# Performance work log

Hardware: AMD Instinct MI355X
Metric: run time of the kernel (lower is better)

## Reference

```python
import jax, jax.numpy as jnp
import numpy as np

NUM_PAPERS = 500000
NUM_AUTHORS = 200000
NUM_EDGES = 2000000
NUM_LABEL_EDGES = 500000
FEAT = 128
HID = 128


def setup_inputs() -> dict:
    key = jax.random.key(0)
    ks = jax.random.split(key, 9)
    paper_x = jax.random.normal(ks[0], (NUM_PAPERS, FEAT), dtype=jnp.float32)
    author_ids = jax.random.randint(ks[1], (NUM_EDGES,), 0, NUM_AUTHORS, dtype=jnp.int32)
    paper_ids = jax.random.randint(ks[2], (NUM_EDGES,), 0, NUM_PAPERS, dtype=jnp.int32)
    label_author_ids = jax.random.randint(ks[3], (NUM_LABEL_EDGES,), 0, NUM_AUTHORS, dtype=jnp.int32)
    label_paper_ids = jax.random.randint(ks[4], (NUM_LABEL_EDGES,), 0, NUM_PAPERS, dtype=jnp.int32)
    s = 1.0 / np.sqrt(FEAT)
    W_paper = jax.random.normal(ks[5], (FEAT, HID), dtype=jnp.float32) * s
    b_paper = jax.random.normal(ks[6], (HID,), dtype=jnp.float32) * 0.01
    W_author = jax.random.normal(ks[7], (HID, HID), dtype=jnp.float32) * s
    b_author = jax.random.normal(ks[8], (HID,), dtype=jnp.float32) * 0.01
    return {
        'paper_x': paper_x,
        'author_ids': author_ids,
        'paper_ids': paper_ids,
        'label_author_ids': label_author_ids,
        'label_paper_ids': label_paper_ids,
        'W_paper': W_paper,
        'b_paper': b_paper,
        'W_author': W_author,
        'b_author': b_author,
    }


def reference(paper_x, author_ids, paper_ids, label_author_ids, label_paper_ids,
              W_paper, b_paper, W_author, b_author):
    # lin_paper: [num_papers, feat] @ [feat, hid] + bias
    paper_h = paper_x @ W_paper + b_paper
    # gather paper embeddings along 'writes' edges: [num_edges, hid]
    gathered = paper_h[paper_ids]
    # scatter_mean over author ids -> [num_authors, hid]
    sums = jax.ops.segment_sum(gathered, author_ids, num_segments=NUM_AUTHORS)
    counts = jax.ops.segment_sum(jnp.ones((author_ids.shape[0],), dtype=paper_h.dtype),
                                 author_ids, num_segments=NUM_AUTHORS)
    author_h = sums / jnp.maximum(counts, 1.0)[:, None]  # authors with no papers -> 0
    # lin_author
    author_h = author_h @ W_author + b_author
    # Classifier: edgewise dot product on supervision edges -> [num_label_edges]
    pred = jnp.sum(author_h[label_author_ids] * paper_h[label_paper_ids], axis=-1)
    return pred
```

## Files before the change

### kernel.cpp

```cpp
#include <hip/hip_runtime.h>

typedef __attribute__((ext_vector_type(8))) short short8;
typedef __attribute__((ext_vector_type(8))) unsigned short ushort8;
typedef __attribute__((ext_vector_type(4))) unsigned short ushort4_t;
typedef __attribute__((ext_vector_type(4))) float floatx4;

#define NUM_AUTHORS 200000
#define HID 128
#define ABITS 9
#define NB 391
#define CHUNK 8192
#define TPB 32
#define OSTRIDE 136

__device__ __forceinline__ unsigned short f32_to_bf16(float f) {
  union { float f; unsigned int u; } v; v.f = f;
  unsigned int u = v.u;
  u += 0x7FFF + ((u >> 16) & 1);
  return (unsigned short)(u >> 16);
}
__device__ __forceinline__ float bf16_to_f32(unsigned short h) {
  union { unsigned int u; float f; } v; v.u = ((unsigned int)h) << 16; return v.f;
}

__global__ __launch_bounds__(256) void prep_w(
    const float* __restrict__ Wp, const float* __restrict__ Wa,
    unsigned short* __restrict__ WtP, unsigned short* __restrict__ WtA)
{
  const float* W = blockIdx.x ? Wa : Wp;
  unsigned short* Wt = blockIdx.x ? WtA : WtP;
  int t = threadIdx.x;
#pragma unroll
  for (int i = 0; i < 8; ++i) {
    int idx = i * 256 + t;
    int f = idx >> 6;
    int lane = idx & 63;
    int tt = f >> 2, ks = f & 3;
    int m = lane & 15, q = lane >> 4;
    int col = tt * 16 + m;
    int kb = ks * 32 + q * 8;
    ushort8 h;
#pragma unroll
    for (int j = 0; j < 8; ++j) h[j] = f32_to_bf16(W[(size_t)(kb + j) * HID + col]);
    *(ushort8*)&Wt[(size_t)idx * 8] = h;
  }
}

template<bool X_IS_BF16>
__global__ __launch_bounds__(256, 4) void gemm_mfma(
    const void* __restrict__ Xv, const unsigned short* __restrict__ Wfrag,
    const float* __restrict__ bias, const int* __restrict__ counts,
    unsigned short* __restrict__ Y, int M, int nTiles)
{
  __shared__ unsigned short Bs[32 * 64 * 8];
  __shared__ unsigned short Obuf[4 * 16 * OSTRIDE];
  const int t = threadIdx.x;
#pragma unroll
  for (int i = 0; i < 8; ++i) {
    int g = i * 256 + t;
    *(ushort8*)&Bs[(size_t)g * 8] = *(const ushort8*)&Wfrag[(size_t)g * 8];
  }
  __syncthreads();

  const int w = t >> 6;
  const int lane = t & 63;
  const int m = lane & 15;
  const int q = lane >> 4;
  unsigned short* ob = &Obuf[w * 16 * OSTRIDE];

  const int tileBase = blockIdx.x * TPB;

#pragma unroll 1
  for (int i = 0; i < TPB / 4; ++i) {
    const int tile = tileBase + i * 4 + w;
    if (tile >= nTiles) break;
    const int p = tile * 16 + m;
    const bool valid = (p < M);

    short8 xf[4];
    if (X_IS_BF16) {
      const unsigned short* X = (const unsigned short*)Xv;
      const unsigned short* xp = X + (size_t)p * HID + q * 8;
#pragma unroll
      for (int ks = 0; ks < 4; ++ks) {
        if (valid) xf[ks] = *(const short8*)(xp + ks * 32);
        else       xf[ks] = (short8)0;
      }
    } else {
      const float* X = (const float*)Xv;
      const float* xp = X + (size_t)p * HID + q * 8;
#pragma unroll
      for (int ks = 0; ks < 4; ++ks) {
        float4 a0, a1;
        if (valid) {
          a0 = *(const float4*)(xp + ks * 32);
          a1 = *(const float4*)(xp + ks * 32 + 4);
        } else {
          a0 = make_float4(0.f, 0.f, 0.f, 0.f); a1 = a0;
        }
        short8 h;
        h[0] = (short)f32_to_bf16(a0.x); h[1] = (short)f32_to_bf16(a0.y);
        h[2] = (short)f32_to_bf16(a0.z); h[3] = (short)f32_to_bf16(a0.w);
        h[4] = (short)f32_to_bf16(a1.x); h[5] = (short)f32_to_bf16(a1.y);
        h[6] = (short)f32_to_bf16(a1.z); h[7] = (short)f32_to_bf16(a1.w);
        xf[ks] = h;
      }
    }

    floatx4 acc[8];
#pragma unroll
    for (int tt = 0; tt < 8; ++tt) acc[tt] = (floatx4)(0.f);

#pragma unroll
    for (int ks = 0; ks < 4; ++ks) {
#pragma unroll
      for (int tt = 0; tt < 8; ++tt) {
        short8 wf = *(const short8*)&Bs[(size_t)((tt * 4 + ks) * 64 + lane) * 8];
        acc[tt] = __builtin_amdgcn_mfma_f32_16x16x32_bf16(wf, xf[ks], acc[tt], 0, 0, 0);
      }
    }

    float inv = 1.0f;
    if (counts) {
      float c = valid ? (float)counts[p] : 1.0f;
      inv = 1.0f / fmaxf(c, 1.0f);
    }

#pragma unroll
    for (int tt = 0; tt < 8; ++tt) {
      const float4 bv = *(const float4*)(bias + tt * 16 + q * 4);
      ushort4_t o;
      o[0] = f32_to_bf16(acc[tt][0] * inv + bv.x);
      o[1] = f32_to_bf16(acc[tt][1] * inv + bv.y);
      o[2] = f32_to_bf16(acc[tt][2] * inv + bv.z);
      o[3] = f32_to_bf16(acc[tt][3] * inv + bv.w);
      *(ushort4_t*)&ob[m * OSTRIDE + tt * 16 + q * 4] = o;
    }
    asm volatile("s_waitcnt lgkmcnt(0)" ::: "memory");

    {
      const int r = lane & 15;
      const int c = lane >> 4;
      const int row = tile * 16 + r;
#pragma unroll
      for (int j = 0; j < 4; ++j) {
        ushort8 v = *(const ushort8*)&ob[r * OSTRIDE + j * 32 + c * 8];
        if (row < M)
          *(ushort8*)(Y + (size_t)row * HID + j * 32 + c * 8) = v;
      }
    }
    asm volatile("s_waitcnt lgkmcnt(0)" ::: "memory");
  }
}

__global__ __launch_bounds__(256) void hist_kernel(
    const int* __restrict__ aid, int* __restrict__ cnt, int n)
{
  int i = blockIdx.x * 256 + threadIdx.x;
  if (i < n) atomicAdd(&cnt[aid[i]], 1);
}

__global__ __launch_bounds__(256) void scan1(
    const int* __restrict__ cnt, int* __restrict__ offsets,
    int* __restrict__ blockSums, int n)
{
  __shared__ int s[256];
  int t = threadIdx.x;
  int i = blockIdx.x * 256 + t;
  int v = (i < n) ? cnt[i] : 0;
  s[t] = v; __syncthreads();
#pragma unroll
  for (int off = 1; off < 256; off <<= 1) {
    int tv = 0;
    if (t >= off) tv = s[t - off];
    __syncthreads();
    if (t >= off) s[t] += tv;
    __syncthreads();
  }
  if (i < n) offsets[i] = s[t] - v;
  if (t == 255) blockSums[blockIdx.x] = s[255];
}

__global__ __launch_bounds__(1024) void scan2(int* __restrict__ blockSums, int nb)
{
  __shared__ int s[1024];
  int t = threadIdx.x;
  int v = (t < nb) ? blockSums[t] : 0;
  s[t] = v; __syncthreads();
#pragma unroll
  for (int off = 1; off < 1024; off <<= 1) {
    int tv = 0;
    if (t >= off) tv = s[t - off];
    __syncthreads();
    if (t >= off) s[t] += tv;
    __syncthreads();
  }
  if (t < nb) blockSums[t] = s[t] - v;
}

__global__ __launch_bounds__(256) void scan3(
    int* __restrict__ offsets, const int* __restrict__ blockSums, int n)
{
  int i = blockIdx.x * 256 + threadIdx.x;
  if (i < n) offsets[i] += blockSums[blockIdx.x];
}

__global__ __launch_bounds__(256) void bucket_hist(
    const int* __restrict__ aid, int* __restrict__ bcnt, int n)
{
  __shared__ int hist[NB];
  int t = threadIdx.x;
  for (int i = t; i < NB; i += 256) hist[i] = 0;
  __syncthreads();
  int e0 = blockIdx.x * CHUNK;
  int e1 = min(e0 + CHUNK, n);
  for (int e = e0 + t; e < e1; e += 256) atomicAdd(&hist[aid[e] >> ABITS], 1);
  __syncthreads();
  for (int i = t; i < NB; i += 256) {
    int h = hist[i];
    if (h) atomicAdd(&bcnt[i], h);
  }
}

__global__ __launch_bounds__(512) void bucket_scan(
    const int* __restrict__ bcnt, int* __restrict__ boff, int* __restrict__ bcur, int n)
{
  __shared__ int s[512];
  int t = threadIdx.x;
  int v = (t < NB) ? bcnt[t] : 0;
  s[t] = v; __syncthreads();
#pragma unroll
  for (int off = 1; off < 512; off <<= 1) {
    int tv = 0;
    if (t >= off) tv = s[t - off];
    __syncthreads();
    if (t >= off) s[t] += tv;
    __syncthreads();
  }
  if (t < NB) { int e = s[t] - v; boff[t] = e; bcur[t] = e; }
  if (t == 0) boff[NB] = n;
}

__global__ __launch_bounds__(256) void partA(
    const int* __restrict__ aid, const int* __restrict__ pid,
    int* __restrict__ bcur, uint2* __restrict__ pairs, int n)
{
  __shared__ int hist[NB];
  __shared__ int cur[NB];
  int t = threadIdx.x;
  for (int i = t; i < NB; i += 256) hist[i] = 0;
  __syncthreads();
  int e0 = blockIdx.x * CHUNK;
  int e1 = min(e0 + CHUNK, n);
  for (int e = e0 + t; e < e1; e += 256) atomicAdd(&hist[aid[e] >> ABITS], 1);
  __syncthreads();
  for (int i = t; i < NB; i += 256) {
    int h = hist[i];
    cur[i] = h ? atomicAdd(&bcur[i], h) : 0;
  }
  __syncthreads();
  for (int e = e0 + t; e < e1; e += 256) {
    int a = aid[e];
    int pos = atomicAdd(&cur[a >> ABITS], 1);
    pairs[pos] = make_uint2((unsigned)a, (unsigned)pid[e]);
  }
}

__global__ __launch_bounds__(256) void partB(
    const uint2* __restrict__ pairs, const int* __restrict__ boff,
    const int* __restrict__ offsets, int* __restrict__ csr)
{
  __shared__ int lcur[1 << ABITS];
  int b = blockIdx.x;
  int t = threadIdx.x;
  int a0 = b << ABITS;
  for (int i = t; i < (1 << ABITS); i += 256) {
    int g = a0 + i;
    lcur[i] = (g < NUM_AUTHORS) ? offsets[g] : 0;
  }
  __syncthreads();
  int s = boff[b], e = boff[b + 1];
  for (int i = s + t; i < e; i += 256) {
    uint2 pr = pairs[i];
    int pos = atomicAdd(&lcur[pr.x - a0], 1);
    csr[pos] = (int)pr.y;
  }
}

__global__ __launch_bounds__(256) void accumulate_kernel(
    const unsigned short* __restrict__ paper_hb, const int* __restrict__ csr,
    const int* __restrict__ offsets, const int* __restrict__ cnt,
    unsigned short* __restrict__ author_in)
{
  int a = blockIdx.x * 4 + (threadIdx.x >> 6);
  if (a >= NUM_AUTHORS) return;
  int lane = threadIdx.x & 63;
  int sub = lane >> 4;
  int c16 = lane & 15;
  int start = offsets[a];
  int n = cnt[a];
  float acc[8];
#pragma unroll
  for (int j = 0; j < 8; ++j) acc[j] = 0.f;
  for (int i = 0; i < n; i += 4) {
    int idx = i + sub;
    if (idx < n) {
      int p = csr[start + idx];
      ushort8 h = *(const ushort8*)(paper_hb + (size_t)p * HID + c16 * 8);
#pragma unroll
      for (int j = 0; j < 8; ++j) acc[j] += bf16_to_f32(h[j]);
    }
  }
#pragma unroll
  for (int j = 0; j < 8; ++j) {
    acc[j] += __shfl_xor(acc[j], 16, 64);
    acc[j] += __shfl_xor(acc[j], 32, 64);
  }
  if (sub == 0) {
    ushort8 o;
#pragma unroll
    for (int j = 0; j < 8; ++j) o[j] = f32_to_bf16(acc[j]);
    *(ushort8*)(author_in + (size_t)a * HID + c16 * 8) = o;
  }
}

__global__ __launch_bounds__(256) void dot_kernel(
    const unsigned short* __restrict__ author_hb, const unsigned short* __restrict__ paper_hb,
    const int* __restrict__ la, const int* __restrict__ lp,
    float* __restrict__ out, int n)
{
  int e = blockIdx.x * 16 + (threadIdx.x >> 4);
  if (e >= n) return;
  int c16 = threadIdx.x & 15;
  int a = la[e], p = lp[e];
  ushort8 ah = *(const ushort8*)(author_hb + (size_t)a * HID + c16 * 8);
  ushort8 ph = *(const ushort8*)(paper_hb + (size_t)p * HID + c16 * 8);
  float s = 0.f;
#pragma unroll
  for (int j = 0; j < 8; ++j) s += bf16_to_f32(ah[j]) * bf16_to_f32(ph[j]);
  s += __shfl_xor(s, 1, 64);
  s += __shfl_xor(s, 2, 64);
  s += __shfl_xor(s, 4, 64);
  s += __shfl_xor(s, 8, 64);
  if (c16 == 0) out[e] = s;
}

extern "C" void kernel_launch(void* const* d_in, const int* in_sizes, int n_in,
                              void* d_out, int out_size, void* d_ws, size_t ws_size,
                              hipStream_t stream)
{
  const float* paper_x          = (const float*)d_in[0];
  const int*   author_ids       = (const int*)d_in[1];
  const int*   paper_ids        = (const int*)d_in[2];
  const int*   label_author_ids = (const int*)d_in[3];
  const int*   label_paper_ids  = (const int*)d_in[4];
  const float* W_paper          = (const float*)d_in[5];
  const float* b_paper          = (const float*)d_in[6];
  const float* W_author         = (const float*)d_in[7];
  const float* b_author         = (const float*)d_in[8];
  float* out = (float*)d_out;

  const int num_papers = in_sizes[0] / HID;
  const int num_edges  = in_sizes[1];
  const int num_label  = in_sizes[3];
  const int NA = NUM_AUTHORS;

  char* ws = (char*)d_ws;
  size_t off = 0;
  auto alloc = [&](size_t bytes) { void* p = ws + off; off = (off + bytes + 255) & ~(size_t)255; return p; };
  unsigned short* paper_hb  = (unsigned short*)alloc((size_t)num_papers * HID * 2);
  unsigned short* author_in = (unsigned short*)alloc((size_t)NA * HID * 2);
  unsigned short* author_hb = (unsigned short*)alloc((size_t)NA * HID * 2);
  int* counts_int = (int*)alloc((size_t)NA * 4);
  int* bcnt       = (int*)alloc((size_t)(NB + 1) * 4);
  int* boff       = (int*)alloc((size_t)(NB + 1) * 4);
  int* bcur       = (int*)alloc((size_t)NB * 4);
  int* offsets    = (int*)alloc((size_t)NA * 4);
  int* blockSums  = (int*)alloc(1024 * 4);
  int* csr        = (int*)alloc((size_t)num_edges * 4);
  uint2* pairs    = (uint2*)alloc((size_t)num_edges * 8);
  unsigned short* WtP = (unsigned short*)alloc(HID * HID * 2);
  unsigned short* WtA = (unsigned short*)alloc(HID * HID * 2);

  hipMemsetAsync(counts_int, 0, (size_t)NA * 4, stream);
  hipMemsetAsync(bcnt, 0, (size_t)(NB + 1) * 4, stream);

  prep_w<<<2, 256, 0, stream>>>(W_paper, W_author, WtP, WtA);

  {
    const int nTiles = (num_papers + 15) / 16;
    const int blocks = (nTiles + TPB - 1) / TPB;
    gemm_mfma<false><<<blocks, 256, 0, stream>>>(
        paper_x, WtP, b_paper, nullptr, paper_hb, num_papers, nTiles);
  }

  hist_kernel<<<(num_edges + 255) / 256, 256, 0, stream>>>(author_ids, counts_int, num_edges);

  const int nb = (NA + 255) / 256;
  scan1<<<nb, 256, 0, stream>>>(counts_int, offsets, blockSums, NA);
  scan2<<<1, 1024, 0, stream>>>(blockSums, nb);
  scan3<<<nb, 256, 0, stream>>>(offsets, blockSums, NA);

  const int nchunks = (num_edges + CHUNK - 1) / CHUNK;
  bucket_hist<<<nchunks, 256, 0, stream>>>(author_ids, bcnt, num_edges);
  bucket_scan<<<1, 512, 0, stream>>>(bcnt, boff, bcur, num_edges);
  partA<<<nchunks, 256, 0, stream>>>(author_ids, paper_ids, bcur, pairs, num_edges);
  partB<<<NB, 256, 0, stream>>>(pairs, boff, offsets, csr);

  accumulate_kernel<<<(NA + 3) / 4, 256, 0, stream>>>(
      paper_hb, csr, offsets, counts_int, author_in);

  {
    const int nTiles = (NA + 15) / 16;
    const int blocks = (nTiles + TPB - 1) / TPB;
    gemm_mfma<true><<<blocks, 256, 0, stream>>>(
        author_in, WtA, b_author, counts_int, author_hb, NA, nTiles);
  }

  dot_kernel<<<(num_label + 15) / 16, 256, 0, stream>>>(
      author_hb, paper_hb, label_author_ids, label_paper_ids, out, num_label);
}
```

Before: 737.0 us.

## Merge scan passes, derive bucket offsets from author offsets, persistent GEMM grid, unroll gather

Replaces the three-kernel block-sum scan with a single kernel in which each block reduces the preceding block sums itself. Bucket offsets are now taken directly from the per-author offsets, which removes the separate bucket histogram, bucket scan and memset. The GEMM grid is sized to about 768 blocks, each looping over a contiguous range of tiles, and paper_x is read with nontemporal loads. The accumulate loop issues two gathers per iteration to raise memory-level parallelism, and the final output uses nontemporal stores. In exchange, later blocks of the merged scan redo O(nb) reads of the block sums.

```diff
diff --git a/kernel.cpp b/kernel.cpp
--- a/kernel.cpp
+++ b/kernel.cpp
@@ -10,7 +10,6 @@
 #define ABITS 9
 #define NB 391
 #define CHUNK 8192
-#define TPB 32
 #define OSTRIDE 136
 
 __device__ __forceinline__ unsigned short f32_to_bf16(float f) {
@@ -50,7 +49,7 @@
 __global__ __launch_bounds__(256, 4) void gemm_mfma(
     const void* __restrict__ Xv, const unsigned short* __restrict__ Wfrag,
     const float* __restrict__ bias, const int* __restrict__ counts,
-    unsigned short* __restrict__ Y, int M, int nTiles)
+    unsigned short* __restrict__ Y, int M, int nTiles, int tpb)
 {
   __shared__ unsigned short Bs[32 * 64 * 8];
   __shared__ unsigned short Obuf[4 * 16 * OSTRIDE];
@@ -68,12 +67,11 @@
   const int q = lane >> 4;
   unsigned short* ob = &Obuf[w * 16 * OSTRIDE];
 
-  const int tileBase = blockIdx.x * TPB;
+  const int t0 = blockIdx.x * tpb;
+  const int t1 = min(t0 + tpb, nTiles);
 
 #pragma unroll 1
-  for (int i = 0; i < TPB / 4; ++i) {
-    const int tile = tileBase + i * 4 + w;
-    if (tile >= nTiles) break;
+  for (int tile = t0 + w; tile < t1; tile += 4) {
     const int p = tile * 16 + m;
     const bool valid = (p < M);
 
@@ -91,18 +89,18 @@
       const float* xp = X + (size_t)p * HID + q * 8;
 #pragma unroll
       for (int ks = 0; ks < 4; ++ks) {
-        float4 a0, a1;
+        floatx4 a0, a1;
         if (valid) {
-          a0 = *(const float4*)(xp + ks * 32);
-          a1 = *(const float4*)(xp + ks * 32 + 4);
+          a0 = __builtin_nontemporal_load((const floatx4*)(xp + ks * 32));
+          a1 = __builtin_nontemporal_load((const floatx4*)(xp + ks * 32 + 4));
         } else {
-          a0 = make_float4(0.f, 0.f, 0.f, 0.f); a1 = a0;
+          a0 = (floatx4)(0.f); a1 = (floatx4)(0.f);
         }
         short8 h;
-        h[0] = (short)f32_to_bf16(a0.x); h[1] = (short)f32_to_bf16(a0.y);
-        h[2] = (short)f32_to_bf16(a0.z); h[3] = (short)f32_to_bf16(a0.w);
-        h[4] = (short)f32_to_bf16(a1.x); h[5] = (short)f32_to_bf16(a1.y);
-        h[6] = (short)f32_to_bf16(a1.z); h[7] = (short)f32_to_bf16(a1.w);
+        h[0] = (short)f32_to_bf16(a0[0]); h[1] = (short)f32_to_bf16(a0[1]);
+        h[2] = (short)f32_to_bf16(a0[2]); h[3] = (short)f32_to_bf16(a0[3]);
+        h[4] = (short)f32_to_bf16(a1[0]); h[5] = (short)f32_to_bf16(a1[1]);
+        h[6] = (short)f32_to_bf16(a1[2]); h[7] = (short)f32_to_bf16(a1[3]);
         xf[ks] = h;
       }
     }
@@ -181,64 +179,30 @@
   if (t == 255) blockSums[blockIdx.x] = s[255];
 }
 
-__global__ __launch_bounds__(1024) void scan2(int* __restrict__ blockSums, int nb)
-{
-  __shared__ int s[1024];
-  int t = threadIdx.x;
-  int v = (t < nb) ? blockSums[t] : 0;
-  s[t] = v; __syncthreads();
-#pragma unroll
-  for (int off = 1; off < 1024; off <<= 1) {
-    int tv = 0;
-    if (t >= off) tv = s[t - off];
+__global__ __launch_bounds__(256) void scan3b(
+    int* __restrict__ offsets, const int* __restrict__ blockSums,
+    const int* __restrict__ cnt, int* __restrict__ boff, int* __restrict__ bcur,
+    int n)
+{
+  __shared__ int s[256];
+  const int t = threadIdx.x;
+  const int bid = blockIdx.x;
+  int part = 0;
+  for (int j = t; j < bid; j += 256) part += blockSums[j];
+  s[t] = part; __syncthreads();
+#pragma unroll
+  for (int off = 128; off > 0; off >>= 1) {
+    if (t < off) s[t] += s[t + off];
     __syncthreads();
-    if (t >= off) s[t] += tv;
-    __syncthreads();
-  }
-  if (t < nb) blockSums[t] = s[t] - v;
-}
-
-__global__ __launch_bounds__(256) void scan3(
-    int* __restrict__ offsets, const int* __restrict__ blockSums, int n)
-{
-  int i = blockIdx.x * 256 + threadIdx.x;
-  if (i < n) offsets[i] += blockSums[blockIdx.x];
-}
-
-__global__ __launch_bounds__(256) void bucket_hist(
-    const int* __restrict__ aid, int* __restrict__ bcnt, int n)
-{
-  __shared__ int hist[NB];
-  int t = threadIdx.x;
-  for (int i = t; i < NB; i += 256) hist[i] = 0;
-  __syncthreads();
-  int e0 = blockIdx.x * CHUNK;
-  int e1 = min(e0 + CHUNK, n);
-  for (int e = e0 + t; e < e1; e += 256) atomicAdd(&hist[aid[e] >> ABITS], 1);
-  __syncthreads();
-  for (int i = t; i < NB; i += 256) {
-    int h = hist[i];
-    if (h) atomicAdd(&bcnt[i], h);
-  }
-}
-
-__global__ __launch_bounds__(512) void bucket_scan(
-    const int* __restrict__ bcnt, int* __restrict__ boff, int* __restrict__ bcur, int n)
-{
-  __shared__ int s[512];
-  int t = threadIdx.x;
-  int v = (t < NB) ? bcnt[t] : 0;
-  s[t] = v; __syncthreads();
-#pragma unroll
-  for (int off = 1; off < 512; off <<= 1) {
-    int tv = 0;
-    if (t >= off) tv = s[t - off];
-    __syncthreads();
-    if (t >= off) s[t] += tv;
-    __syncthreads();
-  }
-  if (t < NB) { int e = s[t] - v; boff[t] = e; bcur[t] = e; }
-  if (t == 0) boff[NB] = n;
+  }
+  const int prefix = s[0];
+  const int i = bid * 256 + t;
+  if (i < n) {
+    int fin = offsets[i] + prefix;
+    offsets[i] = fin;
+    if ((i & 511) == 0) { int b = i >> ABITS; boff[b] = fin; bcur[b] = fin; }
+    if (i == n - 1) boff[NB] = fin + cnt[i];
+  }
 }
 
 __global__ __launch_bounds__(256) void partA(
@@ -302,13 +266,22 @@
   float acc[8];
 #pragma unroll
   for (int j = 0; j < 8; ++j) acc[j] = 0.f;
-  for (int i = 0; i < n; i += 4) {
-    int idx = i + sub;
-    if (idx < n) {
-      int p = csr[start + idx];
-      ushort8 h = *(const ushort8*)(paper_hb + (size_t)p * HID + c16 * 8);
-#pragma unroll
-      for (int j = 0; j < 8; ++j) acc[j] += bf16_to_f32(h[j]);
+  for (int i = 0; i < n; i += 8) {
+    int idx0 = i + sub;
+    int idx1 = i + 4 + sub;
+    bool v0 = idx0 < n, v1 = idx1 < n;
+    int p0 = v0 ? csr[start + idx0] : 0;
+    int p1 = v1 ? csr[start + idx1] : 0;
+    ushort8 h0, h1;
+    if (v0) h0 = *(const ushort8*)(paper_hb + (size_t)p0 * HID + c16 * 8);
+    if (v1) h1 = *(const ushort8*)(paper_hb + (size_t)p1 * HID + c16 * 8);
+    if (v0) {
+#pragma unroll
+      for (int j = 0; j < 8; ++j) acc[j] += bf16_to_f32(h0[j]);
+    }
+    if (v1) {
+#pragma unroll
+      for (int j = 0; j < 8; ++j) acc[j] += bf16_to_f32(h1[j]);
     }
   }
 #pragma unroll
@@ -342,7 +315,7 @@
   s += __shfl_xor(s, 2, 64);
   s += __shfl_xor(s, 4, 64);
   s += __shfl_xor(s, 8, 64);
-  if (c16 == 0) out[e] = s;
+  if (c16 == 0) __builtin_nontemporal_store(s, &out[e]);
 }
 
 extern "C" void kernel_launch(void* const* d_in, const int* in_sizes, int n_in,
@@ -372,7 +345,6 @@
   unsigned short* author_in = (unsigned short*)alloc((size_t)NA * HID * 2);
   unsigned short* author_hb = (unsigned short*)alloc((size_t)NA * HID * 2);
   int* counts_int = (int*)alloc((size_t)NA * 4);
-  int* bcnt       = (int*)alloc((size_t)(NB + 1) * 4);
   int* boff       = (int*)alloc((size_t)(NB + 1) * 4);
   int* bcur       = (int*)alloc((size_t)NB * 4);
   int* offsets    = (int*)alloc((size_t)NA * 4);
@@ -383,27 +355,24 @@
   unsigned short* WtA = (unsigned short*)alloc(HID * HID * 2);
 
   hipMemsetAsync(counts_int, 0, (size_t)NA * 4, stream);
-  hipMemsetAsync(bcnt, 0, (size_t)(NB + 1) * 4, stream);
 
   prep_w<<<2, 256, 0, stream>>>(W_paper, W_author, WtP, WtA);
 
   {
     const int nTiles = (num_papers + 15) / 16;
-    const int blocks = (nTiles + TPB - 1) / TPB;
+    int tpb = (nTiles + 767) / 768;
+    int blocks = (nTiles + tpb - 1) / tpb;
     gemm_mfma<false><<<blocks, 256, 0, stream>>>(
-        paper_x, WtP, b_paper, nullptr, paper_hb, num_papers, nTiles);
+        paper_x, WtP, b_paper, nullptr, paper_hb, num_papers, nTiles, tpb);
   }
 
   hist_kernel<<<(num_edges + 255) / 256, 256, 0, stream>>>(author_ids, counts_int, num_edges);
 
   const int nb = (NA + 255) / 256;
   scan1<<<nb, 256, 0, stream>>>(counts_int, offsets, blockSums, NA);
-  scan2<<<1, 1024, 0, stream>>>(blockSums, nb);
-  scan3<<<nb, 256, 0, stream>>>(offsets, blockSums, NA);
+  scan3b<<<nb, 256, 0, stream>>>(offsets, blockSums, counts_int, boff, bcur, NA);
 
   const int nchunks = (num_edges + CHUNK - 1) / CHUNK;
-  bucket_hist<<<nchunks, 256, 0, stream>>>(author_ids, bcnt, num_edges);
-  bucket_scan<<<1, 512, 0, stream>>>(bcnt, boff, bcur, num_edges);
   partA<<<nchunks, 256, 0, stream>>>(author_ids, paper_ids, bcur, pairs, num_edges);
   partB<<<NB, 256, 0, stream>>>(pairs, boff, offsets, csr);
 
@@ -412,9 +381,10 @@
 
   {
     const int nTiles = (NA + 15) / 16;
-    const int blocks = (nTiles + TPB - 1) / TPB;
+    int tpb = (nTiles + 767) / 768;
+    int blocks = (nTiles + tpb - 1) / tpb;
     gemm_mfma<true><<<blocks, 256, 0, stream>>>(
-        author_in, WtA, b_author, counts_int, author_hb, NA, nTiles);
+        author_in, WtA, b_author, counts_int, author_hb, NA, nTiles, tpb);
   }
 
   dot_kernel<<<(num_label + 15) / 16, 256, 0, stream>>>(
```

Result: faster. 670.0 us (-9.1%).

## Pipeline GEMM loads, fuse per-author counting into partition, retune gather and dot kernels

Applied to the files above, without the earlier changes.

The GEMM now sizes its grid persistently at about 768 blocks and double-buffers register loads of the next tile while computing the current one, using nontemporal loads for fp32 input. The global histogram and three-pass scan are removed, and per-author counts and offsets are computed locally inside the bucket partition kernel. The accumulate kernel gives each author 16 lanes and shuffles CSR indices to issue four gathers at once, and the dot kernel handles two label edges per 16-lane group. This cuts kernel launches and atomic traffic and raises memory-level parallelism, at the cost of more register pressure (launch bounds lowered to 3 blocks).

```diff
diff --git a/kernel.cpp b/kernel.cpp
--- a/kernel.cpp
+++ b/kernel.cpp
@@ -10,7 +10,6 @@
 #define ABITS 9
 #define NB 391
 #define CHUNK 8192
-#define TPB 32
 #define OSTRIDE 136
 
 __device__ __forceinline__ unsigned short f32_to_bf16(float f) {
@@ -47,10 +46,10 @@
 }
 
 template<bool X_IS_BF16>
-__global__ __launch_bounds__(256, 4) void gemm_mfma(
+__global__ __launch_bounds__(256, 3) void gemm_mfma(
     const void* __restrict__ Xv, const unsigned short* __restrict__ Wfrag,
     const float* __restrict__ bias, const int* __restrict__ counts,
-    unsigned short* __restrict__ Y, int M, int nTiles)
+    unsigned short* __restrict__ Y, int M, int nTiles, int tpb)
 {
   __shared__ unsigned short Bs[32 * 64 * 8];
   __shared__ unsigned short Obuf[4 * 16 * OSTRIDE];
@@ -68,41 +67,45 @@
   const int q = lane >> 4;
   unsigned short* ob = &Obuf[w * 16 * OSTRIDE];
 
-  const int tileBase = blockIdx.x * TPB;
-
-#pragma unroll 1
-  for (int i = 0; i < TPB / 4; ++i) {
-    const int tile = tileBase + i * 4 + w;
-    if (tile >= nTiles) break;
-    const int p = tile * 16 + m;
-    const bool valid = (p < M);
-
-    short8 xf[4];
-    if (X_IS_BF16) {
+  const int t0 = blockIdx.x * tpb;
+  const int t1 = min(t0 + tpb, nTiles);
+
+  int tile = t0 + w;
+  if (tile >= t1) return;
+
+  auto loadraw = [&](int tl, floatx4* rf, short8* rs) {
+    const int p = tl * 16 + m;
+    const bool v = (p < M);
+    if constexpr (X_IS_BF16) {
       const unsigned short* X = (const unsigned short*)Xv;
       const unsigned short* xp = X + (size_t)p * HID + q * 8;
 #pragma unroll
-      for (int ks = 0; ks < 4; ++ks) {
-        if (valid) xf[ks] = *(const short8*)(xp + ks * 32);
-        else       xf[ks] = (short8)0;
-      }
+      for (int ks = 0; ks < 4; ++ks)
+        rs[ks] = v ? *(const short8*)(xp + ks * 32) : (short8)0;
     } else {
       const float* X = (const float*)Xv;
       const float* xp = X + (size_t)p * HID + q * 8;
 #pragma unroll
       for (int ks = 0; ks < 4; ++ks) {
-        float4 a0, a1;
-        if (valid) {
-          a0 = *(const float4*)(xp + ks * 32);
-          a1 = *(const float4*)(xp + ks * 32 + 4);
-        } else {
-          a0 = make_float4(0.f, 0.f, 0.f, 0.f); a1 = a0;
-        }
+        rf[2 * ks]     = v ? __builtin_nontemporal_load((const floatx4*)(xp + ks * 32))     : (floatx4)(0.f);
+        rf[2 * ks + 1] = v ? __builtin_nontemporal_load((const floatx4*)(xp + ks * 32 + 4)) : (floatx4)(0.f);
+      }
+    }
+  };
+
+  auto compute_store = [&](int tl, const floatx4* rf, const short8* rs) {
+    short8 xf[4];
+    if constexpr (X_IS_BF16) {
+#pragma unroll
+      for (int ks = 0; ks < 4; ++ks) xf[ks] = rs[ks];
+    } else {
+#pragma unroll
+      for (int ks = 0; ks < 4; ++ks) {
         short8 h;
-        h[0] = (short)f32_to_bf16(a0.x); h[1] = (short)f32_to_bf16(a0.y);
-        h[2] = (short)f32_to_bf16(a0.z); h[3] = (short)f32_to_bf16(a0.w);
-        h[4] = (short)f32_to_bf16(a1.x); h[5] = (short)f32_to_bf16(a1.y);
-        h[6] = (short)f32_to_bf16(a1.z); h[7] = (short)f32_to_bf16(a1.w);
+        h[0] = (short)f32_to_bf16(rf[2*ks][0]); h[1] = (short)f32_to_bf16(rf[2*ks][1]);
+        h[2] = (short)f32_to_bf16(rf[2*ks][2]); h[3] = (short)f32_to_bf16(rf[2*ks][3]);
+        h[4] = (short)f32_to_bf16(rf[2*ks+1][0]); h[5] = (short)f32_to_bf16(rf[2*ks+1][1]);
+        h[6] = (short)f32_to_bf16(rf[2*ks+1][2]); h[7] = (short)f32_to_bf16(rf[2*ks+1][3]);
         xf[ks] = h;
       }
     }
@@ -110,7 +113,6 @@
     floatx4 acc[8];
 #pragma unroll
     for (int tt = 0; tt < 8; ++tt) acc[tt] = (floatx4)(0.f);
-
 #pragma unroll
     for (int ks = 0; ks < 4; ++ks) {
 #pragma unroll
@@ -120,6 +122,8 @@
       }
     }
 
+    const int p = tl * 16 + m;
+    const bool valid = (p < M);
     float inv = 1.0f;
     if (counts) {
       float c = valid ? (float)counts[p] : 1.0f;
@@ -141,68 +145,32 @@
     {
       const int r = lane & 15;
       const int c = lane >> 4;
-      const int row = tile * 16 + r;
+      const int row = tl * 16 + r;
 #pragma unroll
       for (int j = 0; j < 4; ++j) {
-        ushort8 v = *(const ushort8*)&ob[r * OSTRIDE + j * 32 + c * 8];
+        ushort8 vv = *(const ushort8*)&ob[r * OSTRIDE + j * 32 + c * 8];
         if (row < M)
-          *(ushort8*)(Y + (size_t)row * HID + j * 32 + c * 8) = v;
+          *(ushort8*)(Y + (size_t)row * HID + j * 32 + c * 8) = vv;
       }
     }
     asm volatile("s_waitcnt lgkmcnt(0)" ::: "memory");
-  }
-}
-
-__global__ __launch_bounds__(256) void hist_kernel(
-    const int* __restrict__ aid, int* __restrict__ cnt, int n)
-{
-  int i = blockIdx.x * 256 + threadIdx.x;
-  if (i < n) atomicAdd(&cnt[aid[i]], 1);
-}
-
-__global__ __launch_bounds__(256) void scan1(
-    const int* __restrict__ cnt, int* __restrict__ offsets,
-    int* __restrict__ blockSums, int n)
-{
-  __shared__ int s[256];
-  int t = threadIdx.x;
-  int i = blockIdx.x * 256 + t;
-  int v = (i < n) ? cnt[i] : 0;
-  s[t] = v; __syncthreads();
-#pragma unroll
-  for (int off = 1; off < 256; off <<= 1) {
-    int tv = 0;
-    if (t >= off) tv = s[t - off];
-    __syncthreads();
-    if (t >= off) s[t] += tv;
-    __syncthreads();
-  }
-  if (i < n) offsets[i] = s[t] - v;
-  if (t == 255) blockSums[blockIdx.x] = s[255];
-}
-
-__global__ __launch_bounds__(1024) void scan2(int* __restrict__ blockSums, int nb)
-{
-  __shared__ int s[1024];
-  int t = threadIdx.x;
-  int v = (t < nb) ? blockSums[t] : 0;
-  s[t] = v; __syncthreads();
-#pragma unroll
-  for (int off = 1; off < 1024; off <<= 1) {
-    int tv = 0;
-    if (t >= off) tv = s[t - off];
-    __syncthreads();
-    if (t >= off) s[t] += tv;
-    __syncthreads();
-  }
-  if (t < nb) blockSums[t] = s[t] - v;
-}
-
-__global__ __launch_bounds__(256) void scan3(
-    int* __restrict__ offsets, const int* __restrict__ blockSums, int n)
-{
-  int i = blockIdx.x * 256 + threadIdx.x;
-  if (i < n) offsets[i] += blockSums[blockIdx.x];
+  };
+
+  floatx4 rfA[8], rfB[8];
+  short8  rsA[4], rsB[4];
+  loadraw(tile, rfA, rsA);
+  while (true) {
+    int nA = tile + 4;
+    if (nA < t1) loadraw(nA, rfB, rsB);
+    compute_store(tile, rfA, rsA);
+    tile = nA;
+    if (tile >= t1) break;
+    int nB = tile + 4;
+    if (nB < t1) loadraw(nB, rfA, rsA);
+    compute_store(tile, rfB, rsB);
+    tile = nB;
+    if (tile >= t1) break;
+  }
 }
 
 __global__ __launch_bounds__(256) void bucket_hist(
@@ -266,20 +234,39 @@
   }
 }
 
-__global__ __launch_bounds__(256) void partB(
+__global__ __launch_bounds__(256) void partB2(
     const uint2* __restrict__ pairs, const int* __restrict__ boff,
-    const int* __restrict__ offsets, int* __restrict__ csr)
-{
+    int* __restrict__ offsets, int* __restrict__ cnt, int* __restrict__ csr)
+{
+  __shared__ int lcnt[1 << ABITS];
+  __shared__ int lscan[256];
   __shared__ int lcur[1 << ABITS];
-  int b = blockIdx.x;
-  int t = threadIdx.x;
-  int a0 = b << ABITS;
-  for (int i = t; i < (1 << ABITS); i += 256) {
-    int g = a0 + i;
-    lcur[i] = (g < NUM_AUTHORS) ? offsets[g] : 0;
-  }
-  __syncthreads();
-  int s = boff[b], e = boff[b + 1];
+  const int b = blockIdx.x;
+  const int t = threadIdx.x;
+  const int a0 = b << ABITS;
+  lcnt[t] = 0; lcnt[t + 256] = 0;
+  __syncthreads();
+  const int s = boff[b], e = boff[b + 1];
+  for (int i = s + t; i < e; i += 256) atomicAdd(&lcnt[pairs[i].x - a0], 1);
+  __syncthreads();
+  const int c0 = lcnt[2 * t], c1 = lcnt[2 * t + 1];
+  const int v = c0 + c1;
+  lscan[t] = v; __syncthreads();
+#pragma unroll
+  for (int off = 1; off < 256; off <<= 1) {
+    int tv = 0;
+    if (t >= off) tv = lscan[t - off];
+    __syncthreads();
+    if (t >= off) lscan[t] += tv;
+    __syncthreads();
+  }
+  const int ex = lscan[t] - v;
+  const int o0 = s + ex, o1 = o0 + c0;
+  lcur[2 * t] = o0; lcur[2 * t + 1] = o1;
+  const int g0 = a0 + 2 * t, g1 = g0 + 1;
+  if (g0 < NUM_AUTHORS) { offsets[g0] = o0; cnt[g0] = c0; }
+  if (g1 < NUM_AUTHORS) { offsets[g1] = o1; cnt[g1] = c1; }
+  __syncthreads();
   for (int i = s + t; i < e; i += 256) {
     uint2 pr = pairs[i];
     int pos = atomicAdd(&lcur[pr.x - a0], 1);
@@ -292,36 +279,51 @@
     const int* __restrict__ offsets, const int* __restrict__ cnt,
     unsigned short* __restrict__ author_in)
 {
-  int a = blockIdx.x * 4 + (threadIdx.x >> 6);
+  const int a = (blockIdx.x * 256 + threadIdx.x) >> 4;
   if (a >= NUM_AUTHORS) return;
-  int lane = threadIdx.x & 63;
-  int sub = lane >> 4;
-  int c16 = lane & 15;
-  int start = offsets[a];
-  int n = cnt[a];
+  const int c16 = threadIdx.x & 15;
+  const int start = offsets[a];
+  const int n = cnt[a];
   float acc[8];
 #pragma unroll
   for (int j = 0; j < 8; ++j) acc[j] = 0.f;
-  for (int i = 0; i < n; i += 4) {
-    int idx = i + sub;
-    if (idx < n) {
-      int p = csr[start + idx];
-      ushort8 h = *(const ushort8*)(paper_hb + (size_t)p * HID + c16 * 8);
-#pragma unroll
-      for (int j = 0; j < 8; ++j) acc[j] += bf16_to_f32(h[j]);
-    }
-  }
-#pragma unroll
-  for (int j = 0; j < 8; ++j) {
-    acc[j] += __shfl_xor(acc[j], 16, 64);
-    acc[j] += __shfl_xor(acc[j], 32, 64);
-  }
-  if (sub == 0) {
-    ushort8 o;
-#pragma unroll
-    for (int j = 0; j < 8; ++j) o[j] = f32_to_bf16(acc[j]);
-    *(ushort8*)(author_in + (size_t)a * HID + c16 * 8) = o;
-  }
+  for (int i = 0; i < n; i += 16) {
+    const int rem = n - i;
+    int idxv = (c16 < rem) ? csr[start + i + c16] : 0;
+#pragma unroll
+    for (int j0 = 0; j0 < 16; j0 += 4) {
+      if (j0 < rem) {
+        int p0 = __shfl(idxv, j0 + 0, 16);
+        int p1 = __shfl(idxv, j0 + 1, 16);
+        int p2 = __shfl(idxv, j0 + 2, 16);
+        int p3 = __shfl(idxv, j0 + 3, 16);
+        bool v1 = (j0 + 1) < rem, v2 = (j0 + 2) < rem, v3 = (j0 + 3) < rem;
+        ushort8 h0, h1, h2, h3;
+        h0 = *(const ushort8*)(paper_hb + (size_t)p0 * HID + c16 * 8);
+        if (v1) h1 = *(const ushort8*)(paper_hb + (size_t)p1 * HID + c16 * 8);
+        if (v2) h2 = *(const ushort8*)(paper_hb + (size_t)p2 * HID + c16 * 8);
+        if (v3) h3 = *(const ushort8*)(paper_hb + (size_t)p3 * HID + c16 * 8);
+#pragma unroll
+        for (int j = 0; j < 8; ++j) acc[j] += bf16_to_f32(h0[j]);
+        if (v1) {
+#pragma unroll
+          for (int j = 0; j < 8; ++j) acc[j] += bf16_to_f32(h1[j]);
+        }
+        if (v2) {
+#pragma unroll
+          for (int j = 0; j < 8; ++j) acc[j] += bf16_to_f32(h2[j]);
+        }
+        if (v3) {
+#pragma unroll
+          for (int j = 0; j < 8; ++j) acc[j] += bf16_to_f32(h3[j]);
+        }
+      }
+    }
+  }
+  ushort8 o;
+#pragma unroll
+  for (int j = 0; j < 8; ++j) o[j] = f32_to_bf16(acc[j]);
+  *(ushort8*)(author_in + (size_t)a * HID + c16 * 8) = o;
 }
 
 __global__ __launch_bounds__(256) void dot_kernel(
@@ -329,20 +331,33 @@
     const int* __restrict__ la, const int* __restrict__ lp,
     float* __restrict__ out, int n)
 {
-  int e = blockIdx.x * 16 + (threadIdx.x >> 4);
-  if (e >= n) return;
-  int c16 = threadIdx.x & 15;
-  int a = la[e], p = lp[e];
-  ushort8 ah = *(const ushort8*)(author_hb + (size_t)a * HID + c16 * 8);
-  ushort8 ph = *(const ushort8*)(paper_hb + (size_t)p * HID + c16 * 8);
-  float s = 0.f;
-#pragma unroll
-  for (int j = 0; j < 8; ++j) s += bf16_to_f32(ah[j]) * bf16_to_f32(ph[j]);
-  s += __shfl_xor(s, 1, 64);
-  s += __shfl_xor(s, 2, 64);
-  s += __shfl_xor(s, 4, 64);
-  s += __shfl_xor(s, 8, 64);
-  if (c16 == 0) out[e] = s;
+  const int g = blockIdx.x * 16 + (threadIdx.x >> 4);
+  const int e0 = 2 * g, e1 = e0 + 1;
+  if (e0 >= n) return;
+  const int c16 = threadIdx.x & 15;
+  const bool has1 = (e1 < n);
+  int a0i = la[e0], p0i = lp[e0];
+  int a1i = has1 ? la[e1] : a0i;
+  int p1i = has1 ? lp[e1] : p0i;
+  ushort8 ah0 = *(const ushort8*)(author_hb + (size_t)a0i * HID + c16 * 8);
+  ushort8 ph0 = *(const ushort8*)(paper_hb  + (size_t)p0i * HID + c16 * 8);
+  ushort8 ah1 = *(const ushort8*)(author_hb + (size_t)a1i * HID + c16 * 8);
+  ushort8 ph1 = *(const ushort8*)(paper_hb  + (size_t)p1i * HID + c16 * 8);
+  float s0 = 0.f, s1 = 0.f;
+#pragma unroll
+  for (int j = 0; j < 8; ++j) {
+    s0 += bf16_to_f32(ah0[j]) * bf16_to_f32(ph0[j]);
+    s1 += bf16_to_f32(ah1[j]) * bf16_to_f32(ph1[j]);
+  }
+#pragma unroll
+  for (int off = 1; off < 16; off <<= 1) {
+    s0 += __shfl_xor(s0, off, 64);
+    s1 += __shfl_xor(s1, off, 64);
+  }
+  if (c16 == 0) {
+    __builtin_nontemporal_store(s0, &out[e0]);
+    if (has1) __builtin_nontemporal_store(s1, &out[e1]);
+  }
 }
 
 extern "C" void kernel_launch(void* const* d_in, const int* in_sizes, int n_in,
@@ -376,47 +391,40 @@
   int* boff       = (int*)alloc((size_t)(NB + 1) * 4);
   int* bcur       = (int*)alloc((size_t)NB * 4);
   int* offsets    = (int*)alloc((size_t)NA * 4);
-  int* blockSums  = (int*)alloc(1024 * 4);
   int* csr        = (int*)alloc((size_t)num_edges * 4);
   uint2* pairs    = (uint2*)alloc((size_t)num_edges * 8);
   unsigned short* WtP = (unsigned short*)alloc(HID * HID * 2);
   unsigned short* WtA = (unsigned short*)alloc(HID * HID * 2);
 
-  hipMemsetAsync(counts_int, 0, (size_t)NA * 4, stream);
   hipMemsetAsync(bcnt, 0, (size_t)(NB + 1) * 4, stream);
 
   prep_w<<<2, 256, 0, stream>>>(W_paper, W_author, WtP, WtA);
 
   {
     const int nTiles = (num_papers + 15) / 16;
-    const int blocks = (nTiles + TPB - 1) / TPB;
+    int tpb = (nTiles + 767) / 768;
+    int blocks = (nTiles + tpb - 1) / tpb;
     gemm_mfma<false><<<blocks, 256, 0, stream>>>(
-        paper_x, WtP, b_paper, nullptr, paper_hb, num_papers, nTiles);
-  }
-
-  hist_kernel<<<(num_edges + 255) / 256, 256, 0, stream>>>(author_ids, counts_int, num_edges);
-
-  const int nb = (NA + 255) / 256;
-  scan1<<<nb, 256, 0, stream>>>(counts_int, offsets, blockSums, NA);
-  scan2<<<1, 1024, 0, stream>>>(blockSums, nb);
-  scan3<<<nb, 256, 0, stream>>>(offsets, blockSums, NA);
+        paper_x, WtP, b_paper, nullptr, paper_hb, num_papers, nTiles, tpb);
+  }
 
   const int nchunks = (num_edges + CHUNK - 1) / CHUNK;
   bucket_hist<<<nchunks, 256, 0, stream>>>(author_ids, bcnt, num_edges);
   bucket_scan<<<1, 512, 0, stream>>>(bcnt, boff, bcur, num_edges);
   partA<<<nchunks, 256, 0, stream>>>(author_ids, paper_ids, bcur, pairs, num_edges);
-  partB<<<NB, 256, 0, stream>>>(pairs, boff, offsets, csr);
-
-  accumulate_kernel<<<(NA + 3) / 4, 256, 0, stream>>>(
+  partB2<<<NB, 256, 0, stream>>>(pairs, boff, offsets, counts_int, csr);
+
+  accumulate_kernel<<<(NA + 15) / 16, 256, 0, stream>>>(
       paper_hb, csr, offsets, counts_int, author_in);
 
   {
     const int nTiles = (NA + 15) / 16;
-    const int blocks = (nTiles + TPB - 1) / TPB;
+    int tpb = (nTiles + 767) / 768;
+    int blocks = (nTiles + tpb - 1) / tpb;
     gemm_mfma<true><<<blocks, 256, 0, stream>>>(
-        author_in, WtA, b_author, counts_int, author_hb, NA, nTiles);
-  }
-
-  dot_kernel<<<(num_label + 15) / 16, 256, 0, stream>>>(
+        author_in, WtA, b_author, counts_int, author_hb, NA, nTiles, tpb);
+  }
+
+  dot_kernel<<<(num_label + 31) / 32, 256, 0, stream>>>(
       author_hb, paper_hb, label_author_ids, label_paper_ids, out, num_label);
 }
```

After: 592.4 us. -19.6%, faster.
